# Optimization experiments

Measured on AMD Instinct MI355X. Metric: run time of the kernel, lower is better.

The kernel has to match this reference:

```python
import jax, jax.numpy as jnp
import numpy as np

N, D = 8192, 256
NUM_CLASSES = 128
MARGIN = 0.2


def setup_inputs() -> dict:
    key = jax.random.key(0)
    k1, k2 = jax.random.split(key)
    embeddings = jax.random.normal(k1, (N, D), dtype=jnp.float32)
    labels = jax.random.randint(k2, (N,), 0, NUM_CLASSES, dtype=jnp.int64)
    return {"embeddings": embeddings, "labels": labels}


def reference(embeddings, labels):
    n = embeddings.shape[0]
    # cosine distance matrix: 1 - cos_sim, clipped to [0, 2]
    norm = jnp.sqrt(jnp.sum(embeddings * embeddings, axis=-1, keepdims=True))
    normed = embeddings / jnp.maximum(norm, 1e-12)
    sim = normed @ normed.T                      # (N, N)
    dist = jnp.clip(1.0 - sim, 0.0, 2.0)

    same = labels[:, None] == labels[None, :]    # (N, N) same-class mask
    eye = jnp.eye(n, dtype=bool)
    cand = same & ~eye                           # valid positives per anchor
    valid = cand.any(axis=1)                     # anchors with >=1 positive
    pos_idx = jnp.argmax(cand, axis=1)           # first same-class index != i

    rows = jnp.arange(n)
    d_ap = dist[rows, pos_idx]                   # (N,)

    # semi-hard mining: negatives with d_ap < d < d_ap + margin, fallback hardest
    neg = ~same                                  # different class (self excluded)
    semi = neg & (dist > d_ap[:, None]) & (dist < d_ap[:, None] + MARGIN)
    has_semi = semi.any(axis=1)
    inf = jnp.asarray(jnp.inf, dist.dtype)
    d_semi = jnp.where(semi, dist, inf)
    d_hard = jnp.where(neg, dist, inf)
    neg_idx = jnp.where(has_semi, jnp.argmin(d_semi, axis=1), jnp.argmin(d_hard, axis=1))

    d_an = dist[rows, neg_idx]
    losses = jnp.maximum(d_ap - d_an + MARGIN, 0.0) * valid.astype(dist.dtype)
    cnt = valid.sum().astype(dist.dtype)
    return jnp.where(cnt > 0, losses.sum() / cnt, jnp.zeros((), dist.dtype))
```

## Files before the change

kernel.cpp:

```cpp
#include <hip/hip_runtime.h>
#include <math.h>

#define NN 8192
#define DD 256
#define MARGIN 0.2f
#define SL 16
#define CPS (NN / SL)
#define TILES (CPS / 128)
#define IMAX 0x7fffffff

typedef __attribute__((ext_vector_type(4))) float f32x4;
typedef __attribute__((ext_vector_type(2))) long long2_t;
typedef unsigned int u32;
typedef unsigned short u16;
typedef unsigned char u8;

static __device__ __forceinline__ u8 f2e4m3(float x) {
    float a = fabsf(x);
    a = fminf(a, 448.0f);
    const u32 s = (__float_as_uint(x) >> 31) << 7;
    if (a < 0.015625f) {
        const int m = (int)rintf(a * 512.0f);
        return (u8)(s | m);
    }
    u32 u = __float_as_uint(a);
    u += 0x7FFFF + ((u >> 20) & 1);
    const u32 e = (u >> 23) - 120;
    return (u8)(s | (e << 3) | ((u >> 20) & 7));
}

#define GLOAD16(g, l)                                                             \
    __builtin_amdgcn_global_load_lds(                                             \
        (const __attribute__((address_space(1))) void*)(g),                       \
        (__attribute__((address_space(3))) void*)(l), 16, 0, 0)

static __device__ __forceinline__ void comb2(int& a1, int& a2, int b1, int b2) {
    const int lo = min(a1, b1);
    const int hi = max(a1, b1);
    a2 = min(hi, min(a2, b2));
    a1 = lo;
}

__global__ void kprepclass(const float* __restrict__ emb, const int* __restrict__ labels,
                           u8* __restrict__ E8, float* __restrict__ invn,
                           int* __restrict__ posidx) {
    const int tid = threadIdx.x;
    if (blockIdx.x < 2048) {
        const int wid = tid >> 6, l = tid & 63;
        const int row = blockIdx.x * 4 + wid;
        const float4 v = *(const float4*)&emb[(size_t)row * DD + l * 4];
        float ss = v.x * v.x + v.y * v.y + v.z * v.z + v.w * v.w;
#pragma unroll
        for (int o = 1; o < 64; o <<= 1) ss += __shfl_xor(ss, o);
        const float inv = 1.0f / fmaxf(sqrtf(ss), 1e-12f);
        if (l == 0) invn[row] = inv;
        const u32 b0 = f2e4m3(v.x * inv), b1 = f2e4m3(v.y * inv);
        const u32 b2 = f2e4m3(v.z * inv), b3 = f2e4m3(v.w * inv);
        const u32 packed = b0 | (b1 << 8) | (b2 << 16) | (b3 << 24);
        const int kc = l >> 4, h = (l >> 3) & 1, c = (l >> 1) & 3, o = (l & 1) * 4;
        const int g = kc * 64 + c * 16 + h * 8 + o;
        *(u32*)&E8[(size_t)row * DD + g] = packed;
    } else {
        const int c = blockIdx.x - 2048;
        int m1 = IMAX, m2 = IMAX;
        for (int j = tid; j < NN; j += 256) {
            if (labels[j] == c) {
                if (m1 == IMAX) m1 = j;
                else if (m2 == IMAX) m2 = j;
            }
        }
#pragma unroll
        for (int o = 1; o < 64; o <<= 1)
            comb2(m1, m2, __shfl_xor(m1, o), __shfl_xor(m2, o));
        __shared__ int s1[4], s2[4];
        __shared__ int bj1, bj2;
        const int wave = tid >> 6, lane = tid & 63;
        if (lane == 0) { s1[wave] = m1; s2[wave] = m2; }
        __syncthreads();
        if (tid == 0) {
            comb2(m1, m2, s1[1], s2[1]);
            comb2(m1, m2, s1[2], s2[2]);
            comb2(m1, m2, s1[3], s2[3]);
            bj1 = m1; bj2 = m2;
        }
        __syncthreads();
        const int j1 = bj1, j2 = bj2;
        for (int j = tid; j < NN; j += 256)
            if (labels[j] == c) posidx[j] = (j2 == IMAX) ? -1 : ((j == j1) ? j2 : j1);
    }
}

__global__ void kdap(const float* __restrict__ emb, const float* __restrict__ invn,
                     const int* __restrict__ posidx, float* __restrict__ dap) {
    const int wid = threadIdx.x >> 6, l = threadIdx.x & 63;
    const int i = blockIdx.x * 4 + wid;
    const int p = posidx[i];
    float dv = 0.0f;
    if (p >= 0) {
        const float4 a = *(const float4*)&emb[(size_t)i * DD + l * 4];
        const float4 b = *(const float4*)&emb[(size_t)p * DD + l * 4];
        float s = a.x * b.x + a.y * b.y + a.z * b.z + a.w * b.w;
#pragma unroll
        for (int o = 1; o < 64; o <<= 1) s += __shfl_xor(s, o);
        const float sim = s * invn[i] * invn[p];
        dv = fminf(fmaxf(1.0f - sim, 0.0f), 2.0f);
    }
    if (l == 0) dap[i] = dv;
}

__global__ __launch_bounds__(256) void kmine(
    const u8* __restrict__ E8, const int* __restrict__ labels,
    const float* __restrict__ dap, float* __restrict__ pM1, float* __restrict__ pMN)
{
    __shared__ __align__(16) u8 As0[128 * 64], As1[128 * 64];
    __shared__ __align__(16) u8 Bs0[128 * 64], Bs1[128 * 64];
    __shared__ __align__(16) int Ls[CPS];
    __shared__ float RedN[2][128], RedS[2][128];

    const int tid = threadIdx.x;
    const int l = tid & 63;
    const int wid = tid >> 6;
    const int wr = wid >> 1;
    const int wc = wid & 1;
    const int slice = blockIdx.x;
    const int a0 = blockIdx.y * 128;

    const int frow = l & 15;
    const int fq = l >> 4;
    const int prd = (fq ^ ((frow >> 1) & 3)) * 16;
    const int csrc = (tid & 3) ^ ((tid >> 3) & 3);

    if (tid < 128) {
        const int4 lv = *(const int4*)&labels[slice * CPS + tid * 4];
        *(int4*)&Ls[tid * 4] = lv;
    }
    int la[4]; float hiv[4];
#pragma unroll
    for (int n = 0; n < 4; ++n) {
        const int ai = a0 + wc * 64 + n * 16 + frow;
        la[n] = labels[ai];
        hiv[n] = 1.0f - dap[ai];
    }

    const char* Ec = (const char*)E8;
    const char* agp = Ec + (size_t)(slice * CPS + (tid >> 2)) * 256 + csrc * 16;
    const char* bgp = Ec + (size_t)(a0        + (tid >> 2)) * 256 + csrc * 16;

#define STAGE(AB, BB, AP, BP) do {                      \
        GLOAD16((AP),         &AB[tid * 16]);           \
        GLOAD16((AP) + 16384, &AB[tid * 16 + 4096]);    \
        GLOAD16((BP),         &BB[tid * 16]);           \
        GLOAD16((BP) + 16384, &BB[tid * 16 + 4096]);    \
    } while (0)

#define COMPUTE(RA, RB, FIRST) do {                                               \
        long2_t a2[4], b2[4];                                                     \
        _Pragma("unroll")                                                         \
        for (int m = 0; m < 4; ++m)                                               \
            a2[m] = *(const long2_t*)&RA[(wr * 64 + m * 16 + frow) * 64 + prd];   \
        _Pragma("unroll")                                                         \
        for (int n = 0; n < 4; ++n)                                               \
            b2[n] = *(const long2_t*)&RB[(wc * 64 + n * 16 + frow) * 64 + prd];   \
        __builtin_amdgcn_s_setprio(1);                                            \
        _Pragma("unroll")                                                         \
        for (int m = 0; m < 4; ++m)                                               \
            _Pragma("unroll")                                                     \
            for (int n = 0; n < 4; ++n)                                           \
                acc[m][n] = __builtin_amdgcn_mfma_f32_16x16x32_fp8_fp8(           \
                    a2[m].x, b2[n].x, (FIRST) ? Zv : acc[m][n], 0, 0, 0);         \
        _Pragma("unroll")                                                         \
        for (int m = 0; m < 4; ++m)                                               \
            _Pragma("unroll")                                                     \
            for (int n = 0; n < 4; ++n)                                           \
                acc[m][n] = __builtin_amdgcn_mfma_f32_16x16x32_fp8_fp8(           \
                    a2[m].y, b2[n].y, acc[m][n], 0, 0, 0);                        \
        __builtin_amdgcn_s_setprio(0);                                            \
    } while (0)

    float mN[4], m1[4];
#pragma unroll
    for (int n = 0; n < 4; ++n) { mN[n] = -INFINITY; m1[n] = -INFINITY; }
    const f32x4 Zv = {0.f, 0.f, 0.f, 0.f};
    f32x4 acc[4][4];

    STAGE(As0, Bs0, agp, bgp);
    asm volatile("s_waitcnt lgkmcnt(0)" ::: "memory");
    __builtin_amdgcn_s_barrier();

#pragma unroll
    for (int t = 0; t < TILES; ++t) {
        const char* at = agp + t * 32768;
        STAGE(As1, Bs1, at + 64, bgp + 64);
        asm volatile("s_waitcnt vmcnt(4)" ::: "memory");
        __builtin_amdgcn_s_barrier();
        COMPUTE(As0, Bs0, true);
        __builtin_amdgcn_s_barrier();
        STAGE(As0, Bs0, at + 128, bgp + 128);
        asm volatile("s_waitcnt vmcnt(4)" ::: "memory");
        __builtin_amdgcn_s_barrier();
        COMPUTE(As1, Bs1, false);
        __builtin_amdgcn_s_barrier();
        STAGE(As1, Bs1, at + 192, bgp + 192);
        asm volatile("s_waitcnt vmcnt(4)" ::: "memory");
        __builtin_amdgcn_s_barrier();
        COMPUTE(As0, Bs0, false);
        __builtin_amdgcn_s_barrier();
        if (t < TILES - 1) {
            STAGE(As0, Bs0, at + 32768, bgp);
            asm volatile("s_waitcnt vmcnt(4)" ::: "memory");
        } else {
            asm volatile("s_waitcnt vmcnt(0)" ::: "memory");
        }
        __builtin_amdgcn_s_barrier();
        COMPUTE(As1, Bs1, false);
        {
            int lcv[16];
#pragma unroll
            for (int m = 0; m < 4; ++m) {
                const int4 v = *(const int4*)&Ls[t * 128 + wr * 64 + m * 16 + fq * 4];
                lcv[m * 4 + 0] = v.x; lcv[m * 4 + 1] = v.y;
                lcv[m * 4 + 2] = v.z; lcv[m * 4 + 3] = v.w;
            }
#pragma unroll
            for (int n = 0; n < 4; ++n) {
#pragma unroll
                for (int m = 0; m < 4; ++m)
#pragma unroll
                    for (int r = 0; r < 4; ++r) {
                        const float sv = acc[m][n][r];
                        const float sel = (lcv[m * 4 + r] != la[n]) ? sv : -INFINITY;
                        mN[n] = fmaxf(mN[n], sel);
                        m1[n] = fmaxf(m1[n], (sel < hiv[n]) ? sel : -INFINITY);
                    }
            }
        }
        __builtin_amdgcn_s_barrier();
    }
#undef STAGE
#undef COMPUTE

#pragma unroll
    for (int n = 0; n < 4; ++n) {
        mN[n] = fmaxf(mN[n], __shfl_xor(mN[n], 16));
        mN[n] = fmaxf(mN[n], __shfl_xor(mN[n], 32));
        m1[n] = fmaxf(m1[n], __shfl_xor(m1[n], 16));
        m1[n] = fmaxf(m1[n], __shfl_xor(m1[n], 32));
    }
    if (fq == 0) {
#pragma unroll
        for (int n = 0; n < 4; ++n) {
            RedN[wr][wc * 64 + n * 16 + frow] = mN[n];
            RedS[wr][wc * 64 + n * 16 + frow] = m1[n];
        }
    }
    __syncthreads();
    if (tid < 128) {
        pMN[slice * NN + a0 + tid] = fmaxf(RedN[0][tid], RedN[1][tid]);
        pM1[slice * NN + a0 + tid] = fmaxf(RedS[0][tid], RedS[1][tid]);
    }
}

__global__ void kcombine(const int* __restrict__ posidx, const float* __restrict__ dap,
                         const float* __restrict__ pM1, const float* __restrict__ pMN,
                         float* __restrict__ partials)
{
    const int i = blockIdx.x * 256 + threadIdx.x;
    float loss = 0.0f, cnt = 0.0f;
    if (posidx[i] >= 0) {
        float s1 = -INFINITY, sN = -INFINITY;
#pragma unroll
        for (int s = 0; s < SL; ++s) {
            s1 = fmaxf(s1, pM1[s * NN + i]);
            sN = fmaxf(sN, pMN[s * NN + i]);
        }
        const float da = dap[i];
        const float lo = 1.0f - da - MARGIN;
        const float M = (s1 > lo) ? s1 : sN;
        const float dan = fminf(fmaxf(1.0f - M, 0.0f), 2.0f);
        loss = fmaxf(da - dan + MARGIN, 0.0f);
        cnt = 1.0f;
    }
#pragma unroll
    for (int off = 1; off < 64; off <<= 1) {
        loss += __shfl_xor(loss, off);
        cnt  += __shfl_xor(cnt, off);
    }
    __shared__ float sl[4], sc[4];
    const int wave = threadIdx.x >> 6, lane = threadIdx.x & 63;
    if (lane == 0) { sl[wave] = loss; sc[wave] = cnt; }
    __syncthreads();
    if (threadIdx.x == 0) {
        partials[blockIdx.x]      = sl[0] + sl[1] + sl[2] + sl[3];
        partials[32 + blockIdx.x] = sc[0] + sc[1] + sc[2] + sc[3];
    }
}

__global__ void kfinal(const float* __restrict__ partials, float* __restrict__ out) {
    const int t = threadIdx.x;
    float L = (t < 32) ? partials[t] : 0.0f;
    float C = (t < 32) ? partials[32 + t] : 0.0f;
#pragma unroll
    for (int off = 1; off < 64; off <<= 1) {
        L += __shfl_xor(L, off);
        C += __shfl_xor(C, off);
    }
    if (t == 0) out[0] = (C > 0.0f) ? (L / C) : 0.0f;
}

extern "C" void kernel_launch(void* const* d_in, const int* in_sizes, int n_in,
                              void* d_out, int out_size, void* d_ws, size_t ws_size,
                              hipStream_t stream) {
    const float* emb  = (const float*)d_in[0];
    const int* labels = (const int*)d_in[1];
    float* out = (float*)d_out;

    char* w = (char*)d_ws;
    u8*    E8   = (u8*)w;                        w += (size_t)NN * DD;
    float* invn = (float*)w;                     w += NN * 4;
    float* dapv = (float*)w;                     w += NN * 4;
    int*   posi = (int*)w;                       w += NN * 4;
    float* pM1  = (float*)w;                     w += (size_t)SL * NN * 4;
    float* pMN  = (float*)w;                     w += (size_t)SL * NN * 4;
    float* parts = (float*)w;

    kprepclass<<<2048 + 128, 256, 0, stream>>>(emb, labels, E8, invn, posi);
    kdap<<<NN / 4, 256, 0, stream>>>(emb, invn, posi, dapv);
    kmine<<<dim3(SL, NN / 128), 256, 0, stream>>>(E8, labels, dapv, pM1, pMN);
    kcombine<<<NN / 256, 256, 0, stream>>>(posi, dapv, pM1, pMN, parts);
    kfinal<<<1, 64, 0, stream>>>(parts, out);
}
```

Baseline: 58.86 us.

## Keep B tile in registers and stage full-K A tiles through shared memory

The anchor-side (B) fp8 fragments for the block's 128 anchors now sit in registers for the whole kernel instead of being re-staged through LDS every K-step. The candidate-side A tile now covers the full 256-byte row per 128-row tile, double-buffered with an XOR swizzle, which cuts the number of barriers and stage phases from four per tile to one. This trades more registers (64 extra VGPRs for breg) and more LDS (64KB) for fewer synchronisations and less redundant B traffic, and lower occupancy is a risk.

```diff
diff --git a/kernel.cpp b/kernel.cpp
--- a/kernel.cpp
+++ b/kernel.cpp
@@ -112,8 +112,7 @@
     const u8* __restrict__ E8, const int* __restrict__ labels,
     const float* __restrict__ dap, float* __restrict__ pM1, float* __restrict__ pMN)
 {
-    __shared__ __align__(16) u8 As0[128 * 64], As1[128 * 64];
-    __shared__ __align__(16) u8 Bs0[128 * 64], Bs1[128 * 64];
+    __shared__ __align__(16) u8 At0[128 * 256], At1[128 * 256];
     __shared__ __align__(16) int Ls[CPS];
     __shared__ float RedN[2][128], RedS[2][128];
 
@@ -127,8 +126,6 @@
 
     const int frow = l & 15;
     const int fq = l >> 4;
-    const int prd = (fq ^ ((frow >> 1) & 3)) * 16;
-    const int csrc = (tid & 3) ^ ((tid >> 3) & 3);
 
     if (tid < 128) {
         const int4 lv = *(const int4*)&labels[slice * CPS + tid * 4];
@@ -141,40 +138,23 @@
         la[n] = labels[ai];
         hiv[n] = 1.0f - dap[ai];
     }
-
     const char* Ec = (const char*)E8;
-    const char* agp = Ec + (size_t)(slice * CPS + (tid >> 2)) * 256 + csrc * 16;
-    const char* bgp = Ec + (size_t)(a0        + (tid >> 2)) * 256 + csrc * 16;
-
-#define STAGE(AB, BB, AP, BP) do {                      \
-        GLOAD16((AP),         &AB[tid * 16]);           \
-        GLOAD16((AP) + 16384, &AB[tid * 16 + 4096]);    \
-        GLOAD16((BP),         &BB[tid * 16]);           \
-        GLOAD16((BP) + 16384, &BB[tid * 16 + 4096]);    \
-    } while (0)
-
-#define COMPUTE(RA, RB, FIRST) do {                                               \
-        long2_t a2[4], b2[4];                                                     \
-        _Pragma("unroll")                                                         \
-        for (int m = 0; m < 4; ++m)                                               \
-            a2[m] = *(const long2_t*)&RA[(wr * 64 + m * 16 + frow) * 64 + prd];   \
-        _Pragma("unroll")                                                         \
-        for (int n = 0; n < 4; ++n)                                               \
-            b2[n] = *(const long2_t*)&RB[(wc * 64 + n * 16 + frow) * 64 + prd];   \
-        __builtin_amdgcn_s_setprio(1);                                            \
-        _Pragma("unroll")                                                         \
-        for (int m = 0; m < 4; ++m)                                               \
-            _Pragma("unroll")                                                     \
-            for (int n = 0; n < 4; ++n)                                           \
-                acc[m][n] = __builtin_amdgcn_mfma_f32_16x16x32_fp8_fp8(           \
-                    a2[m].x, b2[n].x, (FIRST) ? Zv : acc[m][n], 0, 0, 0);         \
-        _Pragma("unroll")                                                         \
-        for (int m = 0; m < 4; ++m)                                               \
-            _Pragma("unroll")                                                     \
-            for (int n = 0; n < 4; ++n)                                           \
-                acc[m][n] = __builtin_amdgcn_mfma_f32_16x16x32_fp8_fp8(           \
-                    a2[m].y, b2[n].y, acc[m][n], 0, 0, 0);                        \
-        __builtin_amdgcn_s_setprio(0);                                            \
+    long2_t breg[4][4];
+#pragma unroll
+    for (int n = 0; n < 4; ++n)
+#pragma unroll
+        for (int kc = 0; kc < 4; ++kc)
+            breg[n][kc] = *(const long2_t*)(Ec +
+                (size_t)(a0 + wc * 64 + n * 16 + frow) * 256 + kc * 64 + fq * 16);
+
+    const char* asrc = Ec + ((size_t)(slice * CPS) + (tid >> 4)) * 256
+                          + (((tid & 15) ^ (tid >> 4)) * 16);
+
+#define STAGE(BUF, OFF) do {                                    \
+        _Pragma("unroll")                                       \
+        for (int i = 0; i < 8; ++i)                             \
+            GLOAD16(asrc + (OFF) + i * 4096,                    \
+                    &BUF[tid * 16 + i * 4096]);                 \
     } while (0)
 
     float mN[4], m1[4];
@@ -183,61 +163,78 @@
     const f32x4 Zv = {0.f, 0.f, 0.f, 0.f};
     f32x4 acc[4][4];
 
-    STAGE(As0, Bs0, agp, bgp);
+#define COMPTILE(BUF, T) do {                                                       \
+        _Pragma("unroll")                                                           \
+        for (int kc = 0; kc < 4; ++kc) {                                            \
+            long2_t a2[4];                                                          \
+            _Pragma("unroll")                                                       \
+            for (int m = 0; m < 4; ++m)                                             \
+                a2[m] = *(const long2_t*)&BUF[(wr * 64 + m * 16 + frow) * 256       \
+                                              + ((4 * kc + fq) ^ frow) * 16];      \
+            __builtin_amdgcn_s_setprio(1);                                          \
+            _Pragma("unroll")                                                       \
+            for (int m = 0; m < 4; ++m)                                             \
+                _Pragma("unroll")                                                   \
+                for (int n = 0; n < 4; ++n)                                         \
+                    acc[m][n] = __builtin_amdgcn_mfma_f32_16x16x32_fp8_fp8(         \
+                        a2[m].x, breg[n][kc].x, (kc == 0) ? Zv : acc[m][n],         \
+                        0, 0, 0);                                                   \
+            _Pragma("unroll")                                                       \
+            for (int m = 0; m < 4; ++m)                                             \
+                _Pragma("unroll")                                                   \
+                for (int n = 0; n < 4; ++n)                                         \
+                    acc[m][n] = __builtin_amdgcn_mfma_f32_16x16x32_fp8_fp8(         \
+                        a2[m].y, breg[n][kc].y, acc[m][n], 0, 0, 0);                \
+            __builtin_amdgcn_s_setprio(0);                                          \
+        }                                                                           \
+        {                                                                           \
+            int lcv[16];                                                            \
+            _Pragma("unroll")                                                       \
+            for (int m = 0; m < 4; ++m) {                                           \
+                const int4 v = *(const int4*)&Ls[(T) * 128 + wr * 64 + m * 16       \
+                                                 + fq * 4];                        \
+                lcv[m * 4 + 0] = v.x; lcv[m * 4 + 1] = v.y;                         \
+                lcv[m * 4 + 2] = v.z; lcv[m * 4 + 3] = v.w;                         \
+            }                                                                       \
+            _Pragma("unroll")                                                       \
+            for (int n = 0; n < 4; ++n) {                                           \
+                _Pragma("unroll")                                                   \
+                for (int m = 0; m < 4; ++m)                                         \
+                    _Pragma("unroll")                                               \
+                    for (int r = 0; r < 4; ++r) {                                   \
+                        const float sv = acc[m][n][r];                              \
+                        const float sel = (lcv[m * 4 + r] != la[n]) ? sv            \
+                                                                    : -INFINITY;    \
+                        mN[n] = fmaxf(mN[n], sel);                                  \
+                        m1[n] = fmaxf(m1[n], (sel < hiv[n]) ? sel : -INFINITY);     \
+                    }                                                               \
+            }                                                                       \
+        }                                                                           \
+    } while (0)
+
+    STAGE(At0, 0);
     asm volatile("s_waitcnt lgkmcnt(0)" ::: "memory");
-    __builtin_amdgcn_s_barrier();
-
-#pragma unroll
-    for (int t = 0; t < TILES; ++t) {
-        const char* at = agp + t * 32768;
-        STAGE(As1, Bs1, at + 64, bgp + 64);
-        asm volatile("s_waitcnt vmcnt(4)" ::: "memory");
-        __builtin_amdgcn_s_barrier();
-        COMPUTE(As0, Bs0, true);
-        __builtin_amdgcn_s_barrier();
-        STAGE(As0, Bs0, at + 128, bgp + 128);
-        asm volatile("s_waitcnt vmcnt(4)" ::: "memory");
-        __builtin_amdgcn_s_barrier();
-        COMPUTE(As1, Bs1, false);
-        __builtin_amdgcn_s_barrier();
-        STAGE(As1, Bs1, at + 192, bgp + 192);
-        asm volatile("s_waitcnt vmcnt(4)" ::: "memory");
-        __builtin_amdgcn_s_barrier();
-        COMPUTE(As0, Bs0, false);
-        __builtin_amdgcn_s_barrier();
-        if (t < TILES - 1) {
-            STAGE(As0, Bs0, at + 32768, bgp);
-            asm volatile("s_waitcnt vmcnt(4)" ::: "memory");
-        } else {
-            asm volatile("s_waitcnt vmcnt(0)" ::: "memory");
-        }
-        __builtin_amdgcn_s_barrier();
-        COMPUTE(As1, Bs1, false);
-        {
-            int lcv[16];
-#pragma unroll
-            for (int m = 0; m < 4; ++m) {
-                const int4 v = *(const int4*)&Ls[t * 128 + wr * 64 + m * 16 + fq * 4];
-                lcv[m * 4 + 0] = v.x; lcv[m * 4 + 1] = v.y;
-                lcv[m * 4 + 2] = v.z; lcv[m * 4 + 3] = v.w;
-            }
-#pragma unroll
-            for (int n = 0; n < 4; ++n) {
-#pragma unroll
-                for (int m = 0; m < 4; ++m)
-#pragma unroll
-                    for (int r = 0; r < 4; ++r) {
-                        const float sv = acc[m][n][r];
-                        const float sel = (lcv[m * 4 + r] != la[n]) ? sv : -INFINITY;
-                        mN[n] = fmaxf(mN[n], sel);
-                        m1[n] = fmaxf(m1[n], (sel < hiv[n]) ? sel : -INFINITY);
-                    }
-            }
-        }
-        __builtin_amdgcn_s_barrier();
-    }
+
+    STAGE(At1, 32768);
+    asm volatile("s_waitcnt vmcnt(8)" ::: "memory");
+    __builtin_amdgcn_s_barrier();
+    COMPTILE(At0, 0);
+    __builtin_amdgcn_s_barrier();
+    STAGE(At0, 65536);
+    asm volatile("s_waitcnt vmcnt(8)" ::: "memory");
+    __builtin_amdgcn_s_barrier();
+    COMPTILE(At1, 1);
+    __builtin_amdgcn_s_barrier();
+    STAGE(At1, 98304);
+    asm volatile("s_waitcnt vmcnt(8)" ::: "memory");
+    __builtin_amdgcn_s_barrier();
+    COMPTILE(At0, 2);
+    __builtin_amdgcn_s_barrier();
+    asm volatile("s_waitcnt vmcnt(0)" ::: "memory");
+    __builtin_amdgcn_s_barrier();
+    COMPTILE(At1, 3);
 #undef STAGE
-#undef COMPUTE
+#undef COMPTILE
 
 #pragma unroll
     for (int n = 0; n < 4; ++n) {
@@ -246,6 +243,7 @@
         m1[n] = fmaxf(m1[n], __shfl_xor(m1[n], 16));
         m1[n] = fmaxf(m1[n], __shfl_xor(m1[n], 32));
     }
+    __builtin_amdgcn_s_barrier();
     if (fq == 0) {
 #pragma unroll
         for (int n = 0; n < 4; ++n) {
```

Measured after the change: 58.17 us. About the same (-1.2%).

## Replace LDS-staged block GEMM with per-wave register-resident B and direct global A loads

Applied to the files above, without the earlier changes.

The mining kernel no longer stages 128x128 tiles through shared memory with barriers. Each wave now owns a 64-anchor by 512-candidate slice. It keeps its full 64x256 fp8 B operand in registers and reads A fragments and labels straight from global memory, so the wave needs no LDS or block synchronisation. This removes barrier and LDS traffic, but each wave now reuses less data, global/L2 traffic goes up, and the extra register pressure may lower occupancy.

```diff
diff --git a/kernel.cpp b/kernel.cpp
--- a/kernel.cpp
+++ b/kernel.cpp
@@ -6,7 +6,7 @@
 #define MARGIN 0.2f
 #define SL 16
 #define CPS (NN / SL)
-#define TILES (CPS / 128)
+#define NT (CPS / 64)
 #define IMAX 0x7fffffff
 
 typedef __attribute__((ext_vector_type(4))) float f32x4;
@@ -28,11 +28,6 @@
     const u32 e = (u >> 23) - 120;
     return (u8)(s | (e << 3) | ((u >> 20) & 7));
 }
-
-#define GLOAD16(g, l)                                                             \
-    __builtin_amdgcn_global_load_lds(                                             \
-        (const __attribute__((address_space(1))) void*)(g),                       \
-        (__attribute__((address_space(3))) void*)(l), 16, 0, 0)
 
 static __device__ __forceinline__ void comb2(int& a1, int& a2, int b1, int b2) {
     const int lo = min(a1, b1);
@@ -112,70 +107,33 @@
     const u8* __restrict__ E8, const int* __restrict__ labels,
     const float* __restrict__ dap, float* __restrict__ pM1, float* __restrict__ pMN)
 {
-    __shared__ __align__(16) u8 As0[128 * 64], As1[128 * 64];
-    __shared__ __align__(16) u8 Bs0[128 * 64], Bs1[128 * 64];
-    __shared__ __align__(16) int Ls[CPS];
-    __shared__ float RedN[2][128], RedS[2][128];
-
     const int tid = threadIdx.x;
     const int l = tid & 63;
-    const int wid = tid >> 6;
-    const int wr = wid >> 1;
-    const int wc = wid & 1;
-    const int slice = blockIdx.x;
-    const int a0 = blockIdx.y * 128;
+    const int gw = blockIdx.x * 4 + (tid >> 6);
+    const int slice = gw & 15;
+    const int a0 = (gw >> 4) * 64;
+    const int c0 = slice * CPS;
 
     const int frow = l & 15;
     const int fq = l >> 4;
-    const int prd = (fq ^ ((frow >> 1) & 3)) * 16;
-    const int csrc = (tid & 3) ^ ((tid >> 3) & 3);
-
-    if (tid < 128) {
-        const int4 lv = *(const int4*)&labels[slice * CPS + tid * 4];
-        *(int4*)&Ls[tid * 4] = lv;
-    }
+
+    const char* Ec = (const char*)E8;
+
+    long2_t breg[4][4];
+#pragma unroll
+    for (int n = 0; n < 4; ++n)
+#pragma unroll
+        for (int kc = 0; kc < 4; ++kc)
+            breg[n][kc] = *(const long2_t*)(Ec +
+                (size_t)(a0 + n * 16 + frow) * 256 + kc * 64 + fq * 16);
+
     int la[4]; float hiv[4];
 #pragma unroll
     for (int n = 0; n < 4; ++n) {
-        const int ai = a0 + wc * 64 + n * 16 + frow;
+        const int ai = a0 + n * 16 + frow;
         la[n] = labels[ai];
         hiv[n] = 1.0f - dap[ai];
     }
-
-    const char* Ec = (const char*)E8;
-    const char* agp = Ec + (size_t)(slice * CPS + (tid >> 2)) * 256 + csrc * 16;
-    const char* bgp = Ec + (size_t)(a0        + (tid >> 2)) * 256 + csrc * 16;
-
-#define STAGE(AB, BB, AP, BP) do {                      \
-        GLOAD16((AP),         &AB[tid * 16]);           \
-        GLOAD16((AP) + 16384, &AB[tid * 16 + 4096]);    \
-        GLOAD16((BP),         &BB[tid * 16]);           \
-        GLOAD16((BP) + 16384, &BB[tid * 16 + 4096]);    \
-    } while (0)
-
-#define COMPUTE(RA, RB, FIRST) do {                                               \
-        long2_t a2[4], b2[4];                                                     \
-        _Pragma("unroll")                                                         \
-        for (int m = 0; m < 4; ++m)                                               \
-            a2[m] = *(const long2_t*)&RA[(wr * 64 + m * 16 + frow) * 64 + prd];   \
-        _Pragma("unroll")                                                         \
-        for (int n = 0; n < 4; ++n)                                               \
-            b2[n] = *(const long2_t*)&RB[(wc * 64 + n * 16 + frow) * 64 + prd];   \
-        __builtin_amdgcn_s_setprio(1);                                            \
-        _Pragma("unroll")                                                         \
-        for (int m = 0; m < 4; ++m)                                               \
-            _Pragma("unroll")                                                     \
-            for (int n = 0; n < 4; ++n)                                           \
-                acc[m][n] = __builtin_amdgcn_mfma_f32_16x16x32_fp8_fp8(           \
-                    a2[m].x, b2[n].x, (FIRST) ? Zv : acc[m][n], 0, 0, 0);         \
-        _Pragma("unroll")                                                         \
-        for (int m = 0; m < 4; ++m)                                               \
-            _Pragma("unroll")                                                     \
-            for (int n = 0; n < 4; ++n)                                           \
-                acc[m][n] = __builtin_amdgcn_mfma_f32_16x16x32_fp8_fp8(           \
-                    a2[m].y, b2[n].y, acc[m][n], 0, 0, 0);                        \
-        __builtin_amdgcn_s_setprio(0);                                            \
-    } while (0)
 
     float mN[4], m1[4];
 #pragma unroll
@@ -183,61 +141,50 @@
     const f32x4 Zv = {0.f, 0.f, 0.f, 0.f};
     f32x4 acc[4][4];
 
-    STAGE(As0, Bs0, agp, bgp);
-    asm volatile("s_waitcnt lgkmcnt(0)" ::: "memory");
-    __builtin_amdgcn_s_barrier();
-
-#pragma unroll
-    for (int t = 0; t < TILES; ++t) {
-        const char* at = agp + t * 32768;
-        STAGE(As1, Bs1, at + 64, bgp + 64);
-        asm volatile("s_waitcnt vmcnt(4)" ::: "memory");
-        __builtin_amdgcn_s_barrier();
-        COMPUTE(As0, Bs0, true);
-        __builtin_amdgcn_s_barrier();
-        STAGE(As0, Bs0, at + 128, bgp + 128);
-        asm volatile("s_waitcnt vmcnt(4)" ::: "memory");
-        __builtin_amdgcn_s_barrier();
-        COMPUTE(As1, Bs1, false);
-        __builtin_amdgcn_s_barrier();
-        STAGE(As1, Bs1, at + 192, bgp + 192);
-        asm volatile("s_waitcnt vmcnt(4)" ::: "memory");
-        __builtin_amdgcn_s_barrier();
-        COMPUTE(As0, Bs0, false);
-        __builtin_amdgcn_s_barrier();
-        if (t < TILES - 1) {
-            STAGE(As0, Bs0, at + 32768, bgp);
-            asm volatile("s_waitcnt vmcnt(4)" ::: "memory");
-        } else {
-            asm volatile("s_waitcnt vmcnt(0)" ::: "memory");
-        }
-        __builtin_amdgcn_s_barrier();
-        COMPUTE(As1, Bs1, false);
-        {
-            int lcv[16];
-#pragma unroll
-            for (int m = 0; m < 4; ++m) {
-                const int4 v = *(const int4*)&Ls[t * 128 + wr * 64 + m * 16 + fq * 4];
-                lcv[m * 4 + 0] = v.x; lcv[m * 4 + 1] = v.y;
-                lcv[m * 4 + 2] = v.z; lcv[m * 4 + 3] = v.w;
-            }
-#pragma unroll
-            for (int n = 0; n < 4; ++n) {
-#pragma unroll
-                for (int m = 0; m < 4; ++m)
-#pragma unroll
-                    for (int r = 0; r < 4; ++r) {
-                        const float sv = acc[m][n][r];
-                        const float sel = (lcv[m * 4 + r] != la[n]) ? sv : -INFINITY;
-                        mN[n] = fmaxf(mN[n], sel);
-                        m1[n] = fmaxf(m1[n], (sel < hiv[n]) ? sel : -INFINITY);
-                    }
-            }
-        }
-        __builtin_amdgcn_s_barrier();
-    }
-#undef STAGE
-#undef COMPUTE
+    for (int ct = 0; ct < NT; ++ct) {
+        const char* abase = Ec + (size_t)(c0 + ct * 64) * 256;
+        int lcv[16];
+#pragma unroll
+        for (int m = 0; m < 4; ++m) {
+            const int4 v = *(const int4*)&labels[c0 + ct * 64 + m * 16 + fq * 4];
+            lcv[m * 4 + 0] = v.x; lcv[m * 4 + 1] = v.y;
+            lcv[m * 4 + 2] = v.z; lcv[m * 4 + 3] = v.w;
+        }
+#pragma unroll
+        for (int kc = 0; kc < 4; ++kc) {
+            long2_t a2[4];
+#pragma unroll
+            for (int m = 0; m < 4; ++m)
+                a2[m] = *(const long2_t*)(abase +
+                    (size_t)(m * 16 + frow) * 256 + kc * 64 + fq * 16);
+            __builtin_amdgcn_s_setprio(1);
+#pragma unroll
+            for (int m = 0; m < 4; ++m)
+#pragma unroll
+                for (int n = 0; n < 4; ++n)
+                    acc[m][n] = __builtin_amdgcn_mfma_f32_16x16x32_fp8_fp8(
+                        a2[m].x, breg[n][kc].x, (kc == 0) ? Zv : acc[m][n], 0, 0, 0);
+#pragma unroll
+            for (int m = 0; m < 4; ++m)
+#pragma unroll
+                for (int n = 0; n < 4; ++n)
+                    acc[m][n] = __builtin_amdgcn_mfma_f32_16x16x32_fp8_fp8(
+                        a2[m].y, breg[n][kc].y, acc[m][n], 0, 0, 0);
+            __builtin_amdgcn_s_setprio(0);
+        }
+#pragma unroll
+        for (int n = 0; n < 4; ++n) {
+#pragma unroll
+            for (int m = 0; m < 4; ++m)
+#pragma unroll
+                for (int r = 0; r < 4; ++r) {
+                    const float sv = acc[m][n][r];
+                    const float sel = (lcv[m * 4 + r] != la[n]) ? sv : -INFINITY;
+                    mN[n] = fmaxf(mN[n], sel);
+                    m1[n] = fmaxf(m1[n], (sel < hiv[n]) ? sel : -INFINITY);
+                }
+        }
+    }
 
 #pragma unroll
     for (int n = 0; n < 4; ++n) {
@@ -249,14 +196,9 @@
     if (fq == 0) {
 #pragma unroll
         for (int n = 0; n < 4; ++n) {
-            RedN[wr][wc * 64 + n * 16 + frow] = mN[n];
-            RedS[wr][wc * 64 + n * 16 + frow] = m1[n];
-        }
-    }
-    __syncthreads();
-    if (tid < 128) {
-        pMN[slice * NN + a0 + tid] = fmaxf(RedN[0][tid], RedN[1][tid]);
-        pM1[slice * NN + a0 + tid] = fmaxf(RedS[0][tid], RedS[1][tid]);
+            pMN[slice * NN + a0 + n * 16 + frow] = mN[n];
+            pM1[slice * NN + a0 + n * 16 + frow] = m1[n];
+        }
     }
 }
 
@@ -325,7 +267,7 @@
 
     kprepclass<<<2048 + 128, 256, 0, stream>>>(emb, labels, E8, invn, posi);
     kdap<<<NN / 4, 256, 0, stream>>>(emb, invn, posi, dapv);
-    kmine<<<dim3(SL, NN / 128), 256, 0, stream>>>(E8, labels, dapv, pM1, pMN);
+    kmine<<<512, 256, 0, stream>>>(E8, labels, dapv, pM1, pMN);
     kcombine<<<NN / 256, 256, 0, stream>>>(posi, dapv, pM1, pMN, parts);
     kfinal<<<1, 64, 0, stream>>>(parts, out);
 }
```

Measured after the change: 64.24 us. 1.09x slower.
